# Performance work log

Measured on AMD Instinct MI355X. Metric: run time of the kernel, lower is better.

## Reference

```python
import jax, jax.numpy as jnp
import numpy as np
from jax import lax

# Sizes
B, N, F = 8, 4096, 64          # clouds, points per cloud, feature dim
RATIO, RADIUS, K = 0.5, 0.2, 64  # fps ratio, ball radius, max_num_neighbors
S = int(N * RATIO)              # sampled centroids per cloud
H1, H2, H3 = 64, 64, 128        # MLP widths


def setup_inputs() -> dict:
    key = jax.random.key(0)
    ks = jax.random.split(key, 6)
    x = jax.random.normal(ks[0], (B * N, F), jnp.float32)
    pos = jax.random.uniform(ks[1], (B * N, 3), jnp.float32)  # unit cube
    batch = (jnp.arange(B * N) // N).astype(jnp.int32)  # equal-size clouds
    W1 = jax.random.normal(ks[2], (F + 3, H1), jnp.float32) * 0.1
    b1 = jnp.zeros((H1,), jnp.float32)
    W2 = jax.random.normal(ks[3], (H1, H2), jnp.float32) * 0.1
    b2 = jnp.zeros((H2,), jnp.float32)
    W3 = jax.random.normal(ks[4], (H2, H3), jnp.float32) * 0.1
    b3 = jnp.zeros((H3,), jnp.float32)
    return dict(x=x, pos=pos, batch=batch, W1=W1, b1=b1, W2=W2, b2=b2, W3=W3, b3=b3)


def fps_indices(pos_b):
    """Farthest point sampling for one cloud. pos_b: [N,3] -> [S] int32 indices."""
    def step(carry, _):
        cur, dmin = carry
        d = jnp.sum((pos_b - pos_b[cur]) ** 2, axis=-1)  # [N]
        dmin = jnp.minimum(dmin, d)
        nxt = jnp.argmax(dmin).astype(jnp.int32)
        return (nxt, dmin), cur
    init = (jnp.int32(0), jnp.full((N,), jnp.inf, jnp.float32))
    (_, _), sel = lax.scan(step, init, None, length=S)
    return sel


def reference(x, pos, batch, W1, b1, W2, b2, W3, b3):
    x3 = x.reshape(B, N, F)
    pos3 = pos.reshape(B, N, 3)
    batch3 = batch.reshape(B, N)

    # fps returns indices only -> no gradient path through sampling
    idx = jax.vmap(fps_indices)(lax.stop_gradient(pos3))  # [B,S]
    bi = jnp.arange(B)[:, None]
    pos_s = pos3[bi, idx]  # [B,S,3] sampled centroids

    # radius ball query: nearest-K within RADIUS (cap = max_num_neighbors)
    d2 = jnp.sum((pos_s[:, :, None, :] - pos3[:, None, :, :]) ** 2, axis=-1)  # [B,S,N]
    neg_d2, nbr = lax.top_k(-d2, K)          # [B,S,K] nearest K per centroid
    valid = (-neg_d2) <= RADIUS * RADIUS     # [B,S,K] inside-ball mask

    # PointNetConv: message = MLP(concat(x_j, pos_j - pos_i)), aggr = max
    gi = jnp.arange(B)[:, None, None]
    x_j = x3[gi, nbr]                          # [B,S,K,F]
    rel = pos3[gi, nbr] - pos_s[:, :, None, :]  # [B,S,K,3]
    h = jnp.concatenate([x_j, rel], axis=-1)    # [B,S,K,F+3]
    h = jax.nn.relu(h @ W1 + b1)
    h = jax.nn.relu(h @ W2 + b2)
    h = jax.nn.relu(h @ W3 + b3)                # [B,S,K,H3]
    h = jnp.where(valid[..., None], h, -jnp.inf)
    # each centroid is its own neighbor (dist 0 <= RADIUS), so max is finite
    out = jnp.max(h, axis=2)                    # [B,S,H3]

    x_out = out.reshape(B * S, H3)
    pos_out = pos_s.reshape(B * S, 3)
    batch_out = batch3[bi, idx].reshape(B * S)
    return x_out, pos_out, batch_out
```

## Files before the change

kernel.cpp:

```cpp
#include <hip/hip_runtime.h>
#include <cstdint>
#include <cstddef>

#define BB 8
#define NN 4096
#define FF 64
#define SS 2048
#define KK 64
#define H1c 64
#define H2c 64
#define H3c 128
#define R2 0.04f
#define CAPQ 304
#define QRANK 5
#define NY1 240

typedef unsigned long long ull;
typedef __attribute__((ext_vector_type(4))) float f32x4;
typedef __attribute__((ext_vector_type(8))) short bf16x8;

__device__ __forceinline__ float d2_exact(float ax, float ay, float az,
                                          float bx, float by, float bz) {
  float dx = __fsub_rn(ax, bx);
  float dy = __fsub_rn(ay, by);
  float dz = __fsub_rn(az, bz);
  return __fadd_rn(__fadd_rn(__fmul_rn(dx, dx), __fmul_rn(dy, dy)), __fmul_rn(dz, dz));
}

__device__ __forceinline__ unsigned short f2bf(float f) {
  unsigned u = __float_as_uint(f);
  return (unsigned short)((u + 0x7fffu + ((u >> 16) & 1u)) >> 16);
}

#define WAVE_MAX_DPP(v)                                                        \
  do {                                                                         \
    v = max(v, __builtin_amdgcn_update_dpp(0, v, 0x111, 0xf, 0xf, true));      \
    v = max(v, __builtin_amdgcn_update_dpp(0, v, 0x112, 0xf, 0xf, true));      \
    v = max(v, __builtin_amdgcn_update_dpp(0, v, 0x114, 0xf, 0xf, true));      \
    v = max(v, __builtin_amdgcn_update_dpp(0, v, 0x118, 0xf, 0xf, true));      \
    v = max(v, __builtin_amdgcn_update_dpp(0, v, 0x142, 0xf, 0xf, true));      \
    v = max(v, __builtin_amdgcn_update_dpp(0, v, 0x143, 0xf, 0xf, true));      \
  } while (0)

__global__ __launch_bounds__(512) void fused_kernel(
    const float* __restrict__ pos, const float* __restrict__ x,
    const float* __restrict__ W1, const float* __restrict__ b1,
    const float* __restrict__ W2, const float* __restrict__ W3,
    const float* __restrict__ b2, const float* __restrict__ b3,
    float* __restrict__ pos_out, float* __restrict__ batch_out,
    unsigned short* __restrict__ y1b, unsigned short* __restrict__ w2p,
    unsigned short* __restrict__ w3p, float* __restrict__ xpln,
    float* __restrict__ ypln, float* __restrict__ zpln,
    float* __restrict__ posw, int* __restrict__ flags, int* __restrict__ ycnt,
    float* __restrict__ x_out) {
  __shared__ __align__(16) char smem[49408];
  __shared__ ull skey[2][8];
  __shared__ float xs[64][65];
  __shared__ __align__(16) unsigned short lw2[4096];
  __shared__ __align__(16) unsigned short lw3[8192];
  __shared__ float w1r[3][64];
  const int tid = threadIdx.x;
  const int lane = tid & 63, wv = tid >> 6;

  if (blockIdx.x < BB) {
    float* plds = (float*)smem;
    const int b = blockIdx.x;
    const float4* src = (const float4*)(pos + (size_t)b * NN * 3);
    float4* dstl = (float4*)plds;
#pragma unroll
    for (int k = 0; k < 6; ++k) dstl[tid + k * 512] = src[tid + k * 512];
    __syncthreads();

    float px[8], py[8], pz[8], dmin[8];
#pragma unroll
    for (int i = 0; i < 8; ++i) {
      int p = tid * 8 + i;
      px[i] = plds[p * 3 + 0];
      py[i] = plds[p * 3 + 1];
      pz[i] = plds[p * 3 + 2];
      dmin[i] = INFINITY;
    }
    float cx = plds[0], cy = plds[1], cz = plds[2];

    for (int s = 0; s < SS; ++s) {
      if (tid == 0) {
        int o = b * SS + s;
        pos_out[o * 3 + 0] = cx;
        pos_out[o * 3 + 1] = cy;
        pos_out[o * 3 + 2] = cz;
        __hip_atomic_store(&posw[o * 3 + 0], cx, __ATOMIC_RELAXED,
                           __HIP_MEMORY_SCOPE_AGENT);
        __hip_atomic_store(&posw[o * 3 + 1], cy, __ATOMIC_RELAXED,
                           __HIP_MEMORY_SCOPE_AGENT);
        __hip_atomic_store(&posw[o * 3 + 2], cz, __ATOMIC_RELAXED,
                           __HIP_MEMORY_SCOPE_AGENT);
        if ((s & 255) == 255) {
          asm volatile("s_waitcnt vmcnt(0)" ::: "memory");
          __hip_atomic_store(&flags[b * 8 + (s >> 8)], 1, __ATOMIC_RELAXED,
                             __HIP_MEMORY_SCOPE_AGENT);
        }
      }
#pragma unroll
      for (int i = 0; i < 8; ++i) {
        float d = d2_exact(px[i], py[i], pz[i], cx, cy, cz);
        dmin[i] = fminf(dmin[i], d);
      }
      float m0 = fmaxf(fmaxf(dmin[0], dmin[1]), fmaxf(dmin[2], dmin[3]));
      float m1 = fmaxf(fmaxf(dmin[4], dmin[5]), fmaxf(dmin[6], dmin[7]));
      const float lmax = fmaxf(m0, m1);
      int lidx = 0;
#pragma unroll
      for (int i = 7; i >= 0; --i)
        if (__float_as_int(dmin[i]) == __float_as_int(lmax)) lidx = i;

      const int lv = __float_as_int(lmax);
      int v = lv;
      WAVE_MAX_DPP(v);
      const int wmax = __builtin_amdgcn_readlane(v, 63);
      const ull bal = __ballot(lv == wmax);
      const int wl = (int)__builtin_ctzll(bal);
      const int wli = __builtin_amdgcn_readlane(lidx, wl);
      const int widx = ((wv << 6) + wl) * 8 + wli;
      const int buf = s & 1;
      if (lane == 0)
        skey[buf][wv] = ((ull)(unsigned)wmax << 32) | (unsigned)(~widx);
      __syncthreads();

      ull ka = skey[buf][0];
#pragma unroll
      for (int q = 1; q < 8; ++q) {
        ull kq = skey[buf][q];
        if (kq > ka) ka = kq;
      }
      const int cur = (int)(~(unsigned)(ka & 0xffffffffu));
      cx = plds[cur * 3 + 0];
      cy = plds[cur * 3 + 1];
      cz = plds[cur * 3 + 2];
    }
    for (int i = tid; i < SS; i += 512) batch_out[b * SS + i] = (float)b;
    return;
  }

  if (blockIdx.x == BB) {
    for (int e = tid; e < 4096; e += 512) {
      int j = e & 7, l = (e >> 3) & 63, s = (e >> 9) & 1, c = e >> 10;
      w2p[e] = f2bf(W2[(s * 32 + 8 * (l >> 4) + j) * H2c + c * 16 + (l & 15)]);
    }
    for (int e = tid; e < 8192; e += 512) {
      int j = e & 7, l = (e >> 3) & 63, s = (e >> 9) & 1, c = e >> 10;
      w3p[e] = f2bf(W3[(s * 32 + 8 * (l >> 4) + j) * H3c + c * 16 + (l & 15)]);
    }
    for (int i = tid; i < BB * NN; i += 512) {
      xpln[i] = pos[3 * i + 0];
      ypln[i] = pos[3 * i + 1];
      zpln[i] = pos[3 * i + 2];
    }
    __syncthreads();
    if (tid == 0)
      __hip_atomic_fetch_add(ycnt, 1, __ATOMIC_RELEASE, __HIP_MEMORY_SCOPE_AGENT);
    return;
  }

  const int cid = blockIdx.x - BB - 1;

  for (int t = cid; t < 512; t += NY1) {
    const int r0 = t * 64;
    const float4* src = (const float4*)(x + (size_t)r0 * FF);
#pragma unroll
    for (int q = 0; q < 2; q++) {
      int p = tid + q * 512;
      float4 v = src[p];
      int row = (p * 4) >> 6, col = (p * 4) & 63;
      xs[row][col + 0] = v.x;
      xs[row][col + 1] = v.y;
      xs[row][col + 2] = v.z;
      xs[row][col + 3] = v.w;
    }
    __syncthreads();
    const int c4 = (tid & 15) * 4, kb = (tid >> 4) * 2;
    float acc[2][4];
#pragma unroll
    for (int kq = 0; kq < 2; kq++) {
      acc[kq][0] = b1[c4 + 0];
      acc[kq][1] = b1[c4 + 1];
      acc[kq][2] = b1[c4 + 2];
      acc[kq][3] = b1[c4 + 3];
    }
    for (int f = 0; f < FF; ++f) {
      float4 w = *(const float4*)(W1 + f * H1c + c4);
#pragma unroll
      for (int kq = 0; kq < 2; kq++) {
        float a = xs[kb + kq][f];
        acc[kq][0] += a * w.x;
        acc[kq][1] += a * w.y;
        acc[kq][2] += a * w.z;
        acc[kq][3] += a * w.w;
      }
    }
#pragma unroll
    for (int kq = 0; kq < 2; kq++) {
      ushort4 o;
      o.x = f2bf(acc[kq][0]);
      o.y = f2bf(acc[kq][1]);
      o.z = f2bf(acc[kq][2]);
      o.w = f2bf(acc[kq][3]);
      *(ushort4*)(y1b + (size_t)(r0 + kb + kq) * H1c + c4) = o;
    }
    __syncthreads();
  }
  if (tid == 0)
    __hip_atomic_fetch_add(ycnt, 1, __ATOMIC_RELEASE, __HIP_MEMORY_SCOPE_AGENT);

  while (__hip_atomic_load(ycnt, __ATOMIC_RELAXED, __HIP_MEMORY_SCOPE_AGENT) <
         NY1 + 1)
    __builtin_amdgcn_s_sleep(32);
  if (lane == 0)
    (void)__hip_atomic_load(ycnt, __ATOMIC_ACQUIRE, __HIP_MEMORY_SCOPE_AGENT);
  __syncthreads();

  {
    const uint4* s2 = (const uint4*)w2p;
    uint4* d2v = (uint4*)lw2;
    for (int i = tid; i < 512; i += 512) d2v[i] = s2[i];
    const uint4* s3 = (const uint4*)w3p;
    uint4* d3v = (uint4*)lw3;
    for (int i = tid; i < 1024; i += 512) d3v[i] = s3[i];
    if (tid < 192) w1r[tid / 64][tid % 64] = W1[(64 + tid / 64) * H1c + (tid % 64)];
  }
  __syncthreads();
  const bf16x8* w2f = (const bf16x8*)lw2;
  const bf16x8* w3f = (const bf16x8*)lw3;

  ull(*kc)[CAPQ] = (ull(*)[CAPQ])(smem);
  unsigned short(*h2t)[16][88] = (unsigned short(*)[16][88])(smem + 19456);
  float(*red)[128] = (float(*)[128])(smem + 41984);
  int(*nbl)[64] = (int(*)[64])(smem + 46080);
  float(*cc)[4] = (float(*)[4])(smem + 48128);

  const int lrow = lane & 15, g16 = lane >> 4;

  for (int it = cid; it < 2048; it += NY1) {
    const int k = it >> 8;
    const int rr = it & 255;
    const int b = rr >> 5;
    const int j32 = rr & 31;
    const int g0 = b * SS + k * 256 + j32 * 8;

    while (__hip_atomic_load(&flags[b * 8 + k], __ATOMIC_RELAXED,
                             __HIP_MEMORY_SCOPE_AGENT) == 0)
      __builtin_amdgcn_s_sleep(32);
    asm volatile("" ::: "memory");

    {
      const int g = g0 + wv;
      const float cx = __hip_atomic_load(&posw[g * 3 + 0], __ATOMIC_RELAXED,
                                         __HIP_MEMORY_SCOPE_AGENT);
      const float cy = __hip_atomic_load(&posw[g * 3 + 1], __ATOMIC_RELAXED,
                                         __HIP_MEMORY_SCOPE_AGENT);
      const float cz = __hip_atomic_load(&posw[g * 3 + 2], __ATOMIC_RELAXED,
                                         __HIP_MEMORY_SCOPE_AGENT);
      if (lane == 0) {
        cc[wv][0] = cx;
        cc[wv][1] = cy;
        cc[wv][2] = cz;
      }
      const float4* xp4 = (const float4*)(xpln + (size_t)b * NN);
      const float4* yp4 = (const float4*)(ypln + (size_t)b * NN);
      const float4* zp4 = (const float4*)(zpln + (size_t)b * NN);
      const ull lt = (1ull << lane) - 1ull;
      int cnt = 0;
      for (int t = 0; t < 16; ++t) {
        const int f4 = t * 64 + lane;
        float4 xv = xp4[f4], yv = yp4[f4], zv = zp4[f4];
        const int j0 = f4 * 4;
        float dd[4];
        dd[0] = d2_exact(xv.x, yv.x, zv.x, cx, cy, cz);
        dd[1] = d2_exact(xv.y, yv.y, zv.y, cx, cy, cz);
        dd[2] = d2_exact(xv.z, yv.z, zv.z, cx, cy, cz);
        dd[3] = d2_exact(xv.w, yv.w, zv.w, cx, cy, cz);
#pragma unroll
        for (int e = 0; e < 4; ++e) {
          bool pred = (dd[e] <= R2);
          ull mask = __ballot(pred);
          if (pred) {
            int p = cnt + (int)__popcll(mask & lt);
            if (p < CAPQ)
              kc[wv][p] = ((ull)__float_as_uint(dd[e]) << 32) | (unsigned)(j0 + e);
          }
          cnt += (int)__popcll(mask);
        }
      }
      int M = cnt < CAPQ ? cnt : CAPQ;

      if (M <= 64) {
        nbl[wv][lane] =
            (lane < M) ? (b * NN + (int)(unsigned)(kc[wv][lane] & 0xffffffffu)) : -1;
      } else {
        ull mk[QRANK];
        int rk[QRANK];
#pragma unroll
        for (int q = 0; q < QRANK; q++) {
          int p = lane + q * 64;
          mk[q] = (p < M) ? kc[wv][p] : ~0ull;
          rk[q] = 0;
        }
        int i = 0;
        for (; i + 2 <= M; i += 2) {
          ull ka = kc[wv][i], kb2 = kc[wv][i + 1];
#pragma unroll
          for (int q = 0; q < QRANK; q++)
            rk[q] += (int)(ka < mk[q]) + (int)(kb2 < mk[q]);
        }
        if (i < M) {
          ull ka = kc[wv][i];
#pragma unroll
          for (int q = 0; q < QRANK; q++) rk[q] += (int)(ka < mk[q]);
        }
#pragma unroll
        for (int q = 0; q < QRANK; q++) {
          int p = lane + q * 64;
          if (p < M && rk[q] < KK)
            nbl[wv][rk[q]] = b * NN + (int)(unsigned)(mk[q] & 0xffffffffu);
        }
      }
    }
    __syncthreads();

    const int grp = wv >> 2, lw = wv & 3;
    for (int p = 0; p < 4; ++p) {
      const int ci = p * 2 + grp;
      const int* nl = nbl[ci];
      const float cx = cc[ci][0], cy = cc[ci][1], cz = cc[ci][2];
      const int r = lw * 16 + lrow;
      const int j = nl[r];

      bf16x8 a0 = (bf16x8)0, a1 = (bf16x8)0;
      if (j >= 0) {
        const float rx = pos[j * 3 + 0] - cx;
        const float ry = pos[j * 3 + 1] - cy;
        const float rz = pos[j * 3 + 2] - cz;
        const unsigned short* yr = y1b + (size_t)j * H1c;
        uint4 vlo = *(const uint4*)(yr + 8 * g16);
        uint4 vhi = *(const uint4*)(yr + 32 + 8 * g16);
        const unsigned* plo = (const unsigned*)&vlo;
        const unsigned* phi = (const unsigned*)&vhi;
#pragma unroll
        for (int q = 0; q < 4; ++q) {
          unsigned u = plo[q];
          int k0 = 8 * g16 + 2 * q;
          float e0 = __uint_as_float(u << 16) + rx * w1r[0][k0] + ry * w1r[1][k0] +
                     rz * w1r[2][k0];
          float e1 = __uint_as_float(u & 0xffff0000u) + rx * w1r[0][k0 + 1] +
                     ry * w1r[1][k0 + 1] + rz * w1r[2][k0 + 1];
          a0[2 * q] = (short)f2bf(fmaxf(e0, 0.f));
          a0[2 * q + 1] = (short)f2bf(fmaxf(e1, 0.f));
          unsigned u2 = phi[q];
          int k1 = 32 + k0;
          float f0 = __uint_as_float(u2 << 16) + rx * w1r[0][k1] + ry * w1r[1][k1] +
                     rz * w1r[2][k1];
          float f1 = __uint_as_float(u2 & 0xffff0000u) + rx * w1r[0][k1 + 1] +
                     ry * w1r[1][k1 + 1] + rz * w1r[2][k1 + 1];
          a1[2 * q] = (short)f2bf(fmaxf(f0, 0.f));
          a1[2 * q + 1] = (short)f2bf(fmaxf(f1, 0.f));
        }
      }

#pragma unroll
      for (int c = 0; c < 4; ++c) {
        float bb = b2[c * 16 + lrow];
        f32x4 acc = {bb, bb, bb, bb};
        acc = __builtin_amdgcn_mfma_f32_16x16x32_bf16(a0, w2f[(c * 2 + 0) * 64 + lane], acc, 0, 0, 0);
        acc = __builtin_amdgcn_mfma_f32_16x16x32_bf16(a1, w2f[(c * 2 + 1) * 64 + lane], acc, 0, 0, 0);
#pragma unroll
        for (int t = 0; t < 4; ++t)
          h2t[wv][4 * g16 + t][c * 16 + lrow] = f2bf(fmaxf(acc[t], 0.f));
      }

      bf16x8 a20 = *(const bf16x8*)&h2t[wv][lrow][8 * g16];
      bf16x8 a21 = *(const bf16x8*)&h2t[wv][lrow][32 + 8 * g16];

      float vmax[8];
#pragma unroll
      for (int c = 0; c < 8; ++c) {
        float bb = b3[c * 16 + lrow];
        f32x4 acc = {bb, bb, bb, bb};
        acc = __builtin_amdgcn_mfma_f32_16x16x32_bf16(a20, w3f[(c * 2 + 0) * 64 + lane], acc, 0, 0, 0);
        acc = __builtin_amdgcn_mfma_f32_16x16x32_bf16(a21, w3f[(c * 2 + 1) * 64 + lane], acc, 0, 0, 0);
        float m = -INFINITY;
#pragma unroll
        for (int t = 0; t < 4; ++t) {
          int rg = lw * 16 + 4 * g16 + t;
          float val = (nl[rg] >= 0) ? fmaxf(acc[t], 0.f) : -INFINITY;
          m = fmaxf(m, val);
        }
        m = fmaxf(m, __shfl_xor(m, 16));
        m = fmaxf(m, __shfl_xor(m, 32));
        vmax[c] = m;
      }
      if (g16 == 0) {
#pragma unroll
        for (int c = 0; c < 8; ++c) red[wv][c * 16 + lrow] = vmax[c];
      }
      __syncthreads();
      if (tid < 256) {
        const int which = tid >> 7, col = tid & 127;
        const float* rb = red[which * 4];
        float m = fmaxf(fmaxf(rb[col], rb[128 + col]),
                        fmaxf(rb[256 + col], rb[384 + col]));
        x_out[(size_t)(g0 + p * 2 + which) * H3c + col] = m;
      }
      __syncthreads();
    }
  }
}

extern "C" void kernel_launch(void* const* d_in, const int* in_sizes, int n_in,
                              void* d_out, int out_size, void* d_ws, size_t ws_size,
                              hipStream_t stream) {
  const float* x = (const float*)d_in[0];
  const float* pos = (const float*)d_in[1];
  const float* W1 = (const float*)d_in[3];
  const float* b1 = (const float*)d_in[4];
  const float* W2 = (const float*)d_in[5];
  const float* b2 = (const float*)d_in[6];
  const float* W3 = (const float*)d_in[7];
  const float* b3 = (const float*)d_in[8];

  float* out = (float*)d_out;
  float* x_out = out;
  float* pos_out = out + (size_t)BB * SS * H3c;
  float* batch_out = pos_out + (size_t)BB * SS * 3;

  const size_t y1_bytes = (size_t)BB * NN * H1c * sizeof(unsigned short);
  const size_t w2p_bytes = 4096 * sizeof(unsigned short);
  const size_t w3p_bytes = 8192 * sizeof(unsigned short);
  const size_t pln_bytes = (size_t)BB * NN * sizeof(float);
  const size_t posw_bytes = (size_t)BB * SS * 3 * sizeof(float);
  const size_t need =
      y1_bytes + w2p_bytes + w3p_bytes + 3 * pln_bytes + posw_bytes + 512;
  if (ws_size < need) return;
  char* p = (char*)d_ws;
  unsigned short* y1b = (unsigned short*)p;            p += y1_bytes;
  unsigned short* w2p = (unsigned short*)p;            p += w2p_bytes;
  unsigned short* w3p = (unsigned short*)p;            p += w3p_bytes;
  float* xpln = (float*)p;                             p += pln_bytes;
  float* ypln = (float*)p;                             p += pln_bytes;
  float* zpln = (float*)p;                             p += pln_bytes;
  float* posw = (float*)p;                             p += posw_bytes;
  int* flags = (int*)p;
  int* ycnt = flags + 64;

  hipMemsetAsync(flags, 0, 512, stream);
  fused_kernel<<<BB + 1 + NY1, 512, 0, stream>>>(
      pos, x, W1, b1, W2, W3, b2, b3, pos_out, batch_out, y1b, w2p, w3p, xpln,
      ypln, zpln, posw, flags, ycnt, x_out);
}
```

Baseline: 1.228 ms.

## Batch FPS centroid publishing and spin-wait on flags from one thread per block

The FPS blocks stop issuing per-step atomic stores of each centroid and a per-step vmcnt wait. Instead, every 256 steps the whole block copies the finished chunk from pos_out to posw and sets a flag, and the flags are padded onto separate 128-byte lines. Consumer blocks now spin on the ycnt counter and the chunk flags with only thread 0, a longer sleep and a __syncthreads, instead of every wave polling. This is meant to take latency off the serial FPS critical path and cut polling traffic. The cost is an extra block barrier in FPS every 256 steps, and visibility depends on pos_out stores from thread 0 being visible to the other threads after the barrier.

```diff
diff --git a/kernel.cpp b/kernel.cpp
--- a/kernel.cpp
+++ b/kernel.cpp
@@ -88,17 +88,6 @@
         pos_out[o * 3 + 0] = cx;
         pos_out[o * 3 + 1] = cy;
         pos_out[o * 3 + 2] = cz;
-        __hip_atomic_store(&posw[o * 3 + 0], cx, __ATOMIC_RELAXED,
-                           __HIP_MEMORY_SCOPE_AGENT);
-        __hip_atomic_store(&posw[o * 3 + 1], cy, __ATOMIC_RELAXED,
-                           __HIP_MEMORY_SCOPE_AGENT);
-        __hip_atomic_store(&posw[o * 3 + 2], cz, __ATOMIC_RELAXED,
-                           __HIP_MEMORY_SCOPE_AGENT);
-        if ((s & 255) == 255) {
-          asm volatile("s_waitcnt vmcnt(0)" ::: "memory");
-          __hip_atomic_store(&flags[b * 8 + (s >> 8)], 1, __ATOMIC_RELAXED,
-                             __HIP_MEMORY_SCOPE_AGENT);
-        }
       }
 #pragma unroll
       for (int i = 0; i < 8; ++i) {
@@ -136,6 +125,20 @@
       cx = plds[cur * 3 + 0];
       cy = plds[cur * 3 + 1];
       cz = plds[cur * 3 + 2];
+
+      if ((s & 255) == 255) {
+        const int k = s >> 8;
+        const int base = b * SS * 3 + k * 768;
+        for (int i = tid; i < 768; i += 512) {
+          float vv = pos_out[base + i];
+          __hip_atomic_store(&posw[base + i], vv, __ATOMIC_RELAXED,
+                             __HIP_MEMORY_SCOPE_AGENT);
+        }
+        __syncthreads();
+        if (tid == 0)
+          __hip_atomic_store(&flags[(b * 8 + k) * 32], 1, __ATOMIC_RELAXED,
+                             __HIP_MEMORY_SCOPE_AGENT);
+      }
     }
     for (int i = tid; i < SS; i += 512) batch_out[b * SS + i] = (float)b;
     return;
@@ -211,11 +214,12 @@
   if (tid == 0)
     __hip_atomic_fetch_add(ycnt, 1, __ATOMIC_RELEASE, __HIP_MEMORY_SCOPE_AGENT);
 
-  while (__hip_atomic_load(ycnt, __ATOMIC_RELAXED, __HIP_MEMORY_SCOPE_AGENT) <
-         NY1 + 1)
-    __builtin_amdgcn_s_sleep(32);
-  if (lane == 0)
+  if (tid == 0) {
+    while (__hip_atomic_load(ycnt, __ATOMIC_RELAXED, __HIP_MEMORY_SCOPE_AGENT) <
+           NY1 + 1)
+      __builtin_amdgcn_s_sleep(64);
     (void)__hip_atomic_load(ycnt, __ATOMIC_ACQUIRE, __HIP_MEMORY_SCOPE_AGENT);
+  }
   __syncthreads();
 
   {
@@ -246,10 +250,12 @@
     const int j32 = rr & 31;
     const int g0 = b * SS + k * 256 + j32 * 8;
 
-    while (__hip_atomic_load(&flags[b * 8 + k], __ATOMIC_RELAXED,
-                             __HIP_MEMORY_SCOPE_AGENT) == 0)
-      __builtin_amdgcn_s_sleep(32);
-    asm volatile("" ::: "memory");
+    if (tid == 0) {
+      while (__hip_atomic_load(&flags[(b * 8 + k) * 32], __ATOMIC_RELAXED,
+                               __HIP_MEMORY_SCOPE_AGENT) == 0)
+        __builtin_amdgcn_s_sleep(64);
+    }
+    __syncthreads();
 
     {
       const int g = g0 + wv;
@@ -436,8 +442,9 @@
   const size_t w3p_bytes = 8192 * sizeof(unsigned short);
   const size_t pln_bytes = (size_t)BB * NN * sizeof(float);
   const size_t posw_bytes = (size_t)BB * SS * 3 * sizeof(float);
+  const size_t sync_bytes = 64 * 32 * sizeof(int) + 128;
   const size_t need =
-      y1_bytes + w2p_bytes + w3p_bytes + 3 * pln_bytes + posw_bytes + 512;
+      y1_bytes + w2p_bytes + w3p_bytes + 3 * pln_bytes + posw_bytes + sync_bytes;
   if (ws_size < need) return;
   char* p = (char*)d_ws;
   unsigned short* y1b = (unsigned short*)p;            p += y1_bytes;
@@ -448,9 +455,9 @@
   float* zpln = (float*)p;                             p += pln_bytes;
   float* posw = (float*)p;                             p += posw_bytes;
   int* flags = (int*)p;
-  int* ycnt = flags + 64;
-
-  hipMemsetAsync(flags, 0, 512, stream);
+  int* ycnt = flags + 64 * 32;
+
+  hipMemsetAsync(flags, 0, sync_bytes, stream);
   fused_kernel<<<BB + 1 + NY1, 512, 0, stream>>>(
       pos, x, W1, b1, W2, W3, b2, b3, pos_out, batch_out, y1b, w2p, w3p, xpln,
       ypln, zpln, posw, flags, ycnt, x_out);
```

Result: slower. 1.297 ms (+5.6%).

## Offload FPS centroid publishing to a dedicated ninth wave

Applied to the files above, without the earlier changes.

Blocks grow from 512 to 576 threads so that a ninth wave in each FPS block handles the global atomic stores of centroids and progress flags, taking them off the critical path of the eight compute waves. The extra wave publishes each centroid one iteration after it is chosen and signals the final chunk after the loop. Every other code path is guarded to use only the first 512 threads. The cost is an extra wave per block in every role, which may change occupancy and register limits under the new launch bound. Flag publication also lags by one step.

```diff
diff --git a/kernel.cpp b/kernel.cpp
--- a/kernel.cpp
+++ b/kernel.cpp
@@ -42,7 +42,7 @@
     v = max(v, __builtin_amdgcn_update_dpp(0, v, 0x143, 0xf, 0xf, true));      \
   } while (0)
 
-__global__ __launch_bounds__(512) void fused_kernel(
+__global__ __launch_bounds__(576) void fused_kernel(
     const float* __restrict__ pos, const float* __restrict__ x,
     const float* __restrict__ W1, const float* __restrict__ b1,
     const float* __restrict__ W2, const float* __restrict__ W3,
@@ -65,67 +65,74 @@
   if (blockIdx.x < BB) {
     float* plds = (float*)smem;
     const int b = blockIdx.x;
-    const float4* src = (const float4*)(pos + (size_t)b * NN * 3);
-    float4* dstl = (float4*)plds;
-#pragma unroll
-    for (int k = 0; k < 6; ++k) dstl[tid + k * 512] = src[tid + k * 512];
+    if (tid < 512) {
+      const float4* src = (const float4*)(pos + (size_t)b * NN * 3);
+      float4* dstl = (float4*)plds;
+#pragma unroll
+      for (int k = 0; k < 6; ++k) dstl[tid + k * 512] = src[tid + k * 512];
+    }
     __syncthreads();
 
     float px[8], py[8], pz[8], dmin[8];
-#pragma unroll
-    for (int i = 0; i < 8; ++i) {
-      int p = tid * 8 + i;
-      px[i] = plds[p * 3 + 0];
-      py[i] = plds[p * 3 + 1];
-      pz[i] = plds[p * 3 + 2];
-      dmin[i] = INFINITY;
+    if (tid < 512) {
+#pragma unroll
+      for (int i = 0; i < 8; ++i) {
+        int p = tid * 8 + i;
+        px[i] = plds[p * 3 + 0];
+        py[i] = plds[p * 3 + 1];
+        pz[i] = plds[p * 3 + 2];
+        dmin[i] = INFINITY;
+      }
     }
     float cx = plds[0], cy = plds[1], cz = plds[2];
 
     for (int s = 0; s < SS; ++s) {
-      if (tid == 0) {
-        int o = b * SS + s;
-        pos_out[o * 3 + 0] = cx;
-        pos_out[o * 3 + 1] = cy;
-        pos_out[o * 3 + 2] = cz;
+      if (wv < 8) {
+        if (tid == 0) {
+          int o = b * SS + s;
+          pos_out[o * 3 + 0] = cx;
+          pos_out[o * 3 + 1] = cy;
+          pos_out[o * 3 + 2] = cz;
+        }
+#pragma unroll
+        for (int i = 0; i < 8; ++i) {
+          float d = d2_exact(px[i], py[i], pz[i], cx, cy, cz);
+          dmin[i] = fminf(dmin[i], d);
+        }
+        float m0 = fmaxf(fmaxf(dmin[0], dmin[1]), fmaxf(dmin[2], dmin[3]));
+        float m1 = fmaxf(fmaxf(dmin[4], dmin[5]), fmaxf(dmin[6], dmin[7]));
+        const float lmax = fmaxf(m0, m1);
+        int lidx = 0;
+#pragma unroll
+        for (int i = 7; i >= 0; --i)
+          if (__float_as_int(dmin[i]) == __float_as_int(lmax)) lidx = i;
+
+        const int lv = __float_as_int(lmax);
+        int v = lv;
+        WAVE_MAX_DPP(v);
+        const int wmax = __builtin_amdgcn_readlane(v, 63);
+        const ull bal = __ballot(lv == wmax);
+        const int wl = (int)__builtin_ctzll(bal);
+        const int wli = __builtin_amdgcn_readlane(lidx, wl);
+        const int widx = ((wv << 6) + wl) * 8 + wli;
+        if (lane == 0)
+          skey[s & 1][wv] = ((ull)(unsigned)wmax << 32) | (unsigned)(~widx);
+      } else if (lane == 0) {
+        const int o = b * SS + s;
         __hip_atomic_store(&posw[o * 3 + 0], cx, __ATOMIC_RELAXED,
                            __HIP_MEMORY_SCOPE_AGENT);
         __hip_atomic_store(&posw[o * 3 + 1], cy, __ATOMIC_RELAXED,
                            __HIP_MEMORY_SCOPE_AGENT);
         __hip_atomic_store(&posw[o * 3 + 2], cz, __ATOMIC_RELAXED,
                            __HIP_MEMORY_SCOPE_AGENT);
-        if ((s & 255) == 255) {
-          asm volatile("s_waitcnt vmcnt(0)" ::: "memory");
-          __hip_atomic_store(&flags[b * 8 + (s >> 8)], 1, __ATOMIC_RELAXED,
+        if ((s & 255) == 0 && s > 0) {
+          __hip_atomic_store(&flags[b * 8 + (s >> 8) - 1], 1, __ATOMIC_RELAXED,
                              __HIP_MEMORY_SCOPE_AGENT);
         }
       }
-#pragma unroll
-      for (int i = 0; i < 8; ++i) {
-        float d = d2_exact(px[i], py[i], pz[i], cx, cy, cz);
-        dmin[i] = fminf(dmin[i], d);
-      }
-      float m0 = fmaxf(fmaxf(dmin[0], dmin[1]), fmaxf(dmin[2], dmin[3]));
-      float m1 = fmaxf(fmaxf(dmin[4], dmin[5]), fmaxf(dmin[6], dmin[7]));
-      const float lmax = fmaxf(m0, m1);
-      int lidx = 0;
-#pragma unroll
-      for (int i = 7; i >= 0; --i)
-        if (__float_as_int(dmin[i]) == __float_as_int(lmax)) lidx = i;
-
-      const int lv = __float_as_int(lmax);
-      int v = lv;
-      WAVE_MAX_DPP(v);
-      const int wmax = __builtin_amdgcn_readlane(v, 63);
-      const ull bal = __ballot(lv == wmax);
-      const int wl = (int)__builtin_ctzll(bal);
-      const int wli = __builtin_amdgcn_readlane(lidx, wl);
-      const int widx = ((wv << 6) + wl) * 8 + wli;
+      __syncthreads();
+
       const int buf = s & 1;
-      if (lane == 0)
-        skey[buf][wv] = ((ull)(unsigned)wmax << 32) | (unsigned)(~widx);
-      __syncthreads();
-
       ull ka = skey[buf][0];
 #pragma unroll
       for (int q = 1; q < 8; ++q) {
@@ -137,20 +144,26 @@
       cy = plds[cur * 3 + 1];
       cz = plds[cur * 3 + 2];
     }
-    for (int i = tid; i < SS; i += 512) batch_out[b * SS + i] = (float)b;
+    if (wv == 8 && lane == 0) {
+      asm volatile("s_waitcnt vmcnt(0)" ::: "memory");
+      __hip_atomic_store(&flags[b * 8 + 7], 1, __ATOMIC_RELAXED,
+                         __HIP_MEMORY_SCOPE_AGENT);
+    }
+    if (tid < 512)
+      for (int i = tid; i < SS; i += 512) batch_out[b * SS + i] = (float)b;
     return;
   }
 
   if (blockIdx.x == BB) {
-    for (int e = tid; e < 4096; e += 512) {
+    for (int e = tid; e < 4096; e += 576) {
       int j = e & 7, l = (e >> 3) & 63, s = (e >> 9) & 1, c = e >> 10;
       w2p[e] = f2bf(W2[(s * 32 + 8 * (l >> 4) + j) * H2c + c * 16 + (l & 15)]);
     }
-    for (int e = tid; e < 8192; e += 512) {
+    for (int e = tid; e < 8192; e += 576) {
       int j = e & 7, l = (e >> 3) & 63, s = (e >> 9) & 1, c = e >> 10;
       w3p[e] = f2bf(W3[(s * 32 + 8 * (l >> 4) + j) * H3c + c * 16 + (l & 15)]);
     }
-    for (int i = tid; i < BB * NN; i += 512) {
+    for (int i = tid; i < BB * NN; i += 576) {
       xpln[i] = pos[3 * i + 0];
       ypln[i] = pos[3 * i + 1];
       zpln[i] = pos[3 * i + 2];
@@ -165,46 +178,50 @@
 
   for (int t = cid; t < 512; t += NY1) {
     const int r0 = t * 64;
-    const float4* src = (const float4*)(x + (size_t)r0 * FF);
-#pragma unroll
-    for (int q = 0; q < 2; q++) {
-      int p = tid + q * 512;
-      float4 v = src[p];
-      int row = (p * 4) >> 6, col = (p * 4) & 63;
-      xs[row][col + 0] = v.x;
-      xs[row][col + 1] = v.y;
-      xs[row][col + 2] = v.z;
-      xs[row][col + 3] = v.w;
+    if (tid < 512) {
+      const float4* src = (const float4*)(x + (size_t)r0 * FF);
+#pragma unroll
+      for (int q = 0; q < 2; q++) {
+        int p = tid + q * 512;
+        float4 v = src[p];
+        int row = (p * 4) >> 6, col = (p * 4) & 63;
+        xs[row][col + 0] = v.x;
+        xs[row][col + 1] = v.y;
+        xs[row][col + 2] = v.z;
+        xs[row][col + 3] = v.w;
+      }
     }
     __syncthreads();
-    const int c4 = (tid & 15) * 4, kb = (tid >> 4) * 2;
-    float acc[2][4];
-#pragma unroll
-    for (int kq = 0; kq < 2; kq++) {
-      acc[kq][0] = b1[c4 + 0];
-      acc[kq][1] = b1[c4 + 1];
-      acc[kq][2] = b1[c4 + 2];
-      acc[kq][3] = b1[c4 + 3];
-    }
-    for (int f = 0; f < FF; ++f) {
-      float4 w = *(const float4*)(W1 + f * H1c + c4);
+    if (tid < 512) {
+      const int c4 = (tid & 15) * 4, kb = (tid >> 4) * 2;
+      float acc[2][4];
 #pragma unroll
       for (int kq = 0; kq < 2; kq++) {
-        float a = xs[kb + kq][f];
-        acc[kq][0] += a * w.x;
-        acc[kq][1] += a * w.y;
-        acc[kq][2] += a * w.z;
-        acc[kq][3] += a * w.w;
-      }
-    }
-#pragma unroll
-    for (int kq = 0; kq < 2; kq++) {
-      ushort4 o;
-      o.x = f2bf(acc[kq][0]);
-      o.y = f2bf(acc[kq][1]);
-      o.z = f2bf(acc[kq][2]);
-      o.w = f2bf(acc[kq][3]);
-      *(ushort4*)(y1b + (size_t)(r0 + kb + kq) * H1c + c4) = o;
+        acc[kq][0] = b1[c4 + 0];
+        acc[kq][1] = b1[c4 + 1];
+        acc[kq][2] = b1[c4 + 2];
+        acc[kq][3] = b1[c4 + 3];
+      }
+      for (int f = 0; f < FF; ++f) {
+        float4 w = *(const float4*)(W1 + f * H1c + c4);
+#pragma unroll
+        for (int kq = 0; kq < 2; kq++) {
+          float a = xs[kb + kq][f];
+          acc[kq][0] += a * w.x;
+          acc[kq][1] += a * w.y;
+          acc[kq][2] += a * w.z;
+          acc[kq][3] += a * w.w;
+        }
+      }
+#pragma unroll
+      for (int kq = 0; kq < 2; kq++) {
+        ushort4 o;
+        o.x = f2bf(acc[kq][0]);
+        o.y = f2bf(acc[kq][1]);
+        o.z = f2bf(acc[kq][2]);
+        o.w = f2bf(acc[kq][3]);
+        *(ushort4*)(y1b + (size_t)(r0 + kb + kq) * H1c + c4) = o;
+      }
     }
     __syncthreads();
   }
@@ -221,10 +238,10 @@
   {
     const uint4* s2 = (const uint4*)w2p;
     uint4* d2v = (uint4*)lw2;
-    for (int i = tid; i < 512; i += 512) d2v[i] = s2[i];
+    for (int i = tid; i < 512; i += 576) d2v[i] = s2[i];
     const uint4* s3 = (const uint4*)w3p;
     uint4* d3v = (uint4*)lw3;
-    for (int i = tid; i < 1024; i += 512) d3v[i] = s3[i];
+    for (int i = tid; i < 1024; i += 576) d3v[i] = s3[i];
     if (tid < 192) w1r[tid / 64][tid % 64] = W1[(64 + tid / 64) * H1c + (tid % 64)];
   }
   __syncthreads();
@@ -251,7 +268,7 @@
       __builtin_amdgcn_s_sleep(32);
     asm volatile("" ::: "memory");
 
-    {
+    if (wv < 8) {
       const int g = g0 + wv;
       const float cx = __hip_atomic_load(&posw[g * 3 + 0], __ATOMIC_RELAXED,
                                          __HIP_MEMORY_SCOPE_AGENT);
@@ -328,78 +345,80 @@
 
     const int grp = wv >> 2, lw = wv & 3;
     for (int p = 0; p < 4; ++p) {
-      const int ci = p * 2 + grp;
-      const int* nl = nbl[ci];
-      const float cx = cc[ci][0], cy = cc[ci][1], cz = cc[ci][2];
-      const int r = lw * 16 + lrow;
-      const int j = nl[r];
-
-      bf16x8 a0 = (bf16x8)0, a1 = (bf16x8)0;
-      if (j >= 0) {
-        const float rx = pos[j * 3 + 0] - cx;
-        const float ry = pos[j * 3 + 1] - cy;
-        const float rz = pos[j * 3 + 2] - cz;
-        const unsigned short* yr = y1b + (size_t)j * H1c;
-        uint4 vlo = *(const uint4*)(yr + 8 * g16);
-        uint4 vhi = *(const uint4*)(yr + 32 + 8 * g16);
-        const unsigned* plo = (const unsigned*)&vlo;
-        const unsigned* phi = (const unsigned*)&vhi;
-#pragma unroll
-        for (int q = 0; q < 4; ++q) {
-          unsigned u = plo[q];
-          int k0 = 8 * g16 + 2 * q;
-          float e0 = __uint_as_float(u << 16) + rx * w1r[0][k0] + ry * w1r[1][k0] +
-                     rz * w1r[2][k0];
-          float e1 = __uint_as_float(u & 0xffff0000u) + rx * w1r[0][k0 + 1] +
-                     ry * w1r[1][k0 + 1] + rz * w1r[2][k0 + 1];
-          a0[2 * q] = (short)f2bf(fmaxf(e0, 0.f));
-          a0[2 * q + 1] = (short)f2bf(fmaxf(e1, 0.f));
-          unsigned u2 = phi[q];
-          int k1 = 32 + k0;
-          float f0 = __uint_as_float(u2 << 16) + rx * w1r[0][k1] + ry * w1r[1][k1] +
-                     rz * w1r[2][k1];
-          float f1 = __uint_as_float(u2 & 0xffff0000u) + rx * w1r[0][k1 + 1] +
-                     ry * w1r[1][k1 + 1] + rz * w1r[2][k1 + 1];
-          a1[2 * q] = (short)f2bf(fmaxf(f0, 0.f));
-          a1[2 * q + 1] = (short)f2bf(fmaxf(f1, 0.f));
-        }
-      }
-
-#pragma unroll
-      for (int c = 0; c < 4; ++c) {
-        float bb = b2[c * 16 + lrow];
-        f32x4 acc = {bb, bb, bb, bb};
-        acc = __builtin_amdgcn_mfma_f32_16x16x32_bf16(a0, w2f[(c * 2 + 0) * 64 + lane], acc, 0, 0, 0);
-        acc = __builtin_amdgcn_mfma_f32_16x16x32_bf16(a1, w2f[(c * 2 + 1) * 64 + lane], acc, 0, 0, 0);
-#pragma unroll
-        for (int t = 0; t < 4; ++t)
-          h2t[wv][4 * g16 + t][c * 16 + lrow] = f2bf(fmaxf(acc[t], 0.f));
-      }
-
-      bf16x8 a20 = *(const bf16x8*)&h2t[wv][lrow][8 * g16];
-      bf16x8 a21 = *(const bf16x8*)&h2t[wv][lrow][32 + 8 * g16];
-
-      float vmax[8];
-#pragma unroll
-      for (int c = 0; c < 8; ++c) {
-        float bb = b3[c * 16 + lrow];
-        f32x4 acc = {bb, bb, bb, bb};
-        acc = __builtin_amdgcn_mfma_f32_16x16x32_bf16(a20, w3f[(c * 2 + 0) * 64 + lane], acc, 0, 0, 0);
-        acc = __builtin_amdgcn_mfma_f32_16x16x32_bf16(a21, w3f[(c * 2 + 1) * 64 + lane], acc, 0, 0, 0);
-        float m = -INFINITY;
-#pragma unroll
-        for (int t = 0; t < 4; ++t) {
-          int rg = lw * 16 + 4 * g16 + t;
-          float val = (nl[rg] >= 0) ? fmaxf(acc[t], 0.f) : -INFINITY;
-          m = fmaxf(m, val);
-        }
-        m = fmaxf(m, __shfl_xor(m, 16));
-        m = fmaxf(m, __shfl_xor(m, 32));
-        vmax[c] = m;
-      }
-      if (g16 == 0) {
-#pragma unroll
-        for (int c = 0; c < 8; ++c) red[wv][c * 16 + lrow] = vmax[c];
+      if (wv < 8) {
+        const int ci = p * 2 + grp;
+        const int* nl = nbl[ci];
+        const float cx = cc[ci][0], cy = cc[ci][1], cz = cc[ci][2];
+        const int r = lw * 16 + lrow;
+        const int j = nl[r];
+
+        bf16x8 a0 = (bf16x8)0, a1 = (bf16x8)0;
+        if (j >= 0) {
+          const float rx = pos[j * 3 + 0] - cx;
+          const float ry = pos[j * 3 + 1] - cy;
+          const float rz = pos[j * 3 + 2] - cz;
+          const unsigned short* yr = y1b + (size_t)j * H1c;
+          uint4 vlo = *(const uint4*)(yr + 8 * g16);
+          uint4 vhi = *(const uint4*)(yr + 32 + 8 * g16);
+          const unsigned* plo = (const unsigned*)&vlo;
+          const unsigned* phi = (const unsigned*)&vhi;
+#pragma unroll
+          for (int q = 0; q < 4; ++q) {
+            unsigned u = plo[q];
+            int k0 = 8 * g16 + 2 * q;
+            float e0 = __uint_as_float(u << 16) + rx * w1r[0][k0] +
+                       ry * w1r[1][k0] + rz * w1r[2][k0];
+            float e1 = __uint_as_float(u & 0xffff0000u) + rx * w1r[0][k0 + 1] +
+                       ry * w1r[1][k0 + 1] + rz * w1r[2][k0 + 1];
+            a0[2 * q] = (short)f2bf(fmaxf(e0, 0.f));
+            a0[2 * q + 1] = (short)f2bf(fmaxf(e1, 0.f));
+            unsigned u2 = phi[q];
+            int k1 = 32 + k0;
+            float f0 = __uint_as_float(u2 << 16) + rx * w1r[0][k1] +
+                       ry * w1r[1][k1] + rz * w1r[2][k1];
+            float f1 = __uint_as_float(u2 & 0xffff0000u) + rx * w1r[0][k1 + 1] +
+                       ry * w1r[1][k1 + 1] + rz * w1r[2][k1 + 1];
+            a1[2 * q] = (short)f2bf(fmaxf(f0, 0.f));
+            a1[2 * q + 1] = (short)f2bf(fmaxf(f1, 0.f));
+          }
+        }
+
+#pragma unroll
+        for (int c = 0; c < 4; ++c) {
+          float bb = b2[c * 16 + lrow];
+          f32x4 acc = {bb, bb, bb, bb};
+          acc = __builtin_amdgcn_mfma_f32_16x16x32_bf16(a0, w2f[(c * 2 + 0) * 64 + lane], acc, 0, 0, 0);
+          acc = __builtin_amdgcn_mfma_f32_16x16x32_bf16(a1, w2f[(c * 2 + 1) * 64 + lane], acc, 0, 0, 0);
+#pragma unroll
+          for (int t = 0; t < 4; ++t)
+            h2t[wv][4 * g16 + t][c * 16 + lrow] = f2bf(fmaxf(acc[t], 0.f));
+        }
+
+        bf16x8 a20 = *(const bf16x8*)&h2t[wv][lrow][8 * g16];
+        bf16x8 a21 = *(const bf16x8*)&h2t[wv][lrow][32 + 8 * g16];
+
+        float vmax[8];
+#pragma unroll
+        for (int c = 0; c < 8; ++c) {
+          float bb = b3[c * 16 + lrow];
+          f32x4 acc = {bb, bb, bb, bb};
+          acc = __builtin_amdgcn_mfma_f32_16x16x32_bf16(a20, w3f[(c * 2 + 0) * 64 + lane], acc, 0, 0, 0);
+          acc = __builtin_amdgcn_mfma_f32_16x16x32_bf16(a21, w3f[(c * 2 + 1) * 64 + lane], acc, 0, 0, 0);
+          float m = -INFINITY;
+#pragma unroll
+          for (int t = 0; t < 4; ++t) {
+            int rg = lw * 16 + 4 * g16 + t;
+            float val = (nl[rg] >= 0) ? fmaxf(acc[t], 0.f) : -INFINITY;
+            m = fmaxf(m, val);
+          }
+          m = fmaxf(m, __shfl_xor(m, 16));
+          m = fmaxf(m, __shfl_xor(m, 32));
+          vmax[c] = m;
+        }
+        if (g16 == 0) {
+#pragma unroll
+          for (int c = 0; c < 8; ++c) red[wv][c * 16 + lrow] = vmax[c];
+        }
       }
       __syncthreads();
       if (tid < 256) {
@@ -451,7 +470,7 @@
   int* ycnt = flags + 64;
 
   hipMemsetAsync(flags, 0, 512, stream);
-  fused_kernel<<<BB + 1 + NY1, 512, 0, stream>>>(
+  fused_kernel<<<BB + 1 + NY1, 576, 0, stream>>>(
       pos, x, W1, b1, W2, W3, b2, b3, pos_out, batch_out, y1b, w2p, w3p, xpln,
       ypln, zpln, posw, flags, ycnt, x_out);
 }
```

Result: no change. 1.221 ms, median of 2 (-0.6%).
